# Optimization experiments

Hardware: AMD Instinct MI355X
Metric: run time of the kernel (lower is better)

The kernel has to match this reference:

```python
import jax, jax.numpy as jnp
import numpy as np

N_NODES = 35
N_EDGES = 1190
N_VIEWS = 6
C1_IN, C1_OUT = 1, 256
C2_IN, C2_OUT = 256, 256
C3_IN, C3_OUT = 256, 64


def _nnconv(x, edge_attr, src, dst, nn_w, nn_b, lin_w, bias, c_in, c_out):
    """PyG NNConv with aggr='mean': per-edge MLP weight, gather-matvec-scatter."""
    # per-edge weight matrices: [E, c_in, c_out]
    W = jax.nn.relu(edge_attr @ nn_w.T + nn_b).reshape(-1, c_in, c_out)
    # gather source features and apply per-edge weight: [E, c_out]
    msg = jnp.einsum('ei,eio->eo', x[src], W)
    # scatter-mean into target nodes
    agg = jax.ops.segment_sum(msg, dst, num_segments=N_NODES)
    cnt = jax.ops.segment_sum(jnp.ones((msg.shape[0],), msg.dtype), dst,
                              num_segments=N_NODES)
    agg = agg / jnp.maximum(cnt, 1.0)[:, None]
    # root transform (lin has no bias in PyG) + conv bias
    return agg + x @ lin_w.T + bias


def setup_inputs() -> dict:
    key = jax.random.key(0)
    ks = jax.random.split(key, 16)
    s = 0.05
    x = jnp.ones((N_NODES, C1_IN), jnp.float32)
    edge_attr = jax.random.uniform(ks[0], (N_EDGES, N_VIEWS), jnp.float32)
    edge_index = jax.random.randint(ks[1], (2, N_EDGES), 0, N_NODES, jnp.int32)
    inp = {
        'x': x, 'edge_attr': edge_attr, 'edge_index': edge_index,
        'nn1_w': jax.random.normal(ks[2], (C1_IN * C1_OUT, N_VIEWS), jnp.float32) * s,
        'nn1_b': jax.random.normal(ks[3], (C1_IN * C1_OUT,), jnp.float32) * s,
        'lin1_w': jax.random.normal(ks[4], (C1_OUT, C1_IN), jnp.float32) * s,
        'b1': jax.random.normal(ks[5], (C1_OUT,), jnp.float32) * s,
        'nn2_w': jax.random.normal(ks[6], (C2_IN * C2_OUT, N_VIEWS), jnp.float32) * s,
        'nn2_b': jax.random.normal(ks[7], (C2_IN * C2_OUT,), jnp.float32) * s,
        'lin2_w': jax.random.normal(ks[8], (C2_OUT, C2_IN), jnp.float32) * s,
        'b2': jax.random.normal(ks[9], (C2_OUT,), jnp.float32) * s,
        'nn3_w': jax.random.normal(ks[10], (C3_IN * C3_OUT, N_VIEWS), jnp.float32) * s,
        'nn3_b': jax.random.normal(ks[11], (C3_IN * C3_OUT,), jnp.float32) * s,
        'lin3_w': jax.random.normal(ks[12], (C3_OUT, C3_IN), jnp.float32) * s,
        'b3': jax.random.normal(ks[13], (C3_OUT,), jnp.float32) * s,
    }
    return inp


def reference(x, edge_attr, edge_index, nn1_w, nn1_b, lin1_w, b1,
              nn2_w, nn2_b, lin2_w, b2, nn3_w, nn3_b, lin3_w, b3):
    src, dst = edge_index[0], edge_index[1]
    x = jax.nn.relu(_nnconv(x, edge_attr, src, dst, nn1_w, nn1_b, lin1_w, b1, C1_IN, C1_OUT))
    x = jax.nn.relu(_nnconv(x, edge_attr, src, dst, nn2_w, nn2_b, lin2_w, b2, C2_IN, C2_OUT))
    x = jax.nn.relu(_nnconv(x, edge_attr, src, dst, nn3_w, nn3_b, lin3_w, b3, C3_IN, C3_OUT))
    # CBT: pairwise L1 distances over feature dim -> [N, N]
    # (equivalent to repeat(35,1,1) / transpose / abs / sum since N == 35)
    cbt = jnp.abs(x[None, :, :] - x[:, None, :]).sum(-1)
    return cbt
```

## Files before the change

### kernel.cpp

```cpp
#include <hip/hip_runtime.h>


#define NN 35
#define NE 1190
#define NBLK 224
#define MAXE 96

#define OFF_CNT  320
#define OFF_EL   384
#define OFF_X1   3840
#define OFF_X2   12800
#define OFF_X3   21760
#define OFF_AGG3 24064

__global__ __launch_bounds__(64) void init_k(unsigned* bar) {
    for (int i = threadIdx.x; i < 320; i += 64) bar[i] = 0u;
}

__device__ __forceinline__ float ld_c(const float* p) {
    return __hip_atomic_load(p, __ATOMIC_RELAXED, __HIP_MEMORY_SCOPE_AGENT);
}
__device__ __forceinline__ void st_c(float* p, float v) {
    __hip_atomic_store(p, v, __ATOMIC_RELAXED, __HIP_MEMORY_SCOPE_AGENT);
}
__device__ __forceinline__ int ld_ci(const int* p) {
    return __hip_atomic_load(p, __ATOMIC_RELAXED, __HIP_MEMORY_SCOPE_AGENT);
}
__device__ __forceinline__ void st_ci(int* p, int v) {
    __hip_atomic_store(p, v, __ATOMIC_RELAXED, __HIP_MEMORY_SCOPE_AGENT);
}
__device__ __forceinline__ float2 ld_c2(const float* p) {
    union { double d; float2 f; } u;
    u.d = __hip_atomic_load((const double*)p, __ATOMIC_RELAXED,
                            __HIP_MEMORY_SCOPE_AGENT);
    return u.f;
}
__device__ __forceinline__ void st_c2(float* p, float2 v) {
    union { double d; float2 f; } u;
    u.f = v;
    __hip_atomic_store((double*)p, u.d, __ATOMIC_RELAXED,
                       __HIP_MEMORY_SCOPE_AGENT);
}

__device__ __forceinline__ void gbar(unsigned* bar, unsigned target) {
    __syncthreads();
    if (threadIdx.x == 0) {
        __hip_atomic_fetch_add(bar + (blockIdx.x & 15) * 16, 1u,
                               __ATOMIC_RELAXED, __HIP_MEMORY_SCOPE_AGENT);
        for (;;) {
            unsigned s = 0;
#pragma unroll
            for (int i = 0; i < 16; i++)
                s += __hip_atomic_load(bar + i * 16, __ATOMIC_RELAXED,
                                       __HIP_MEMORY_SCOPE_AGENT);
            if (s >= target) break;
            __builtin_amdgcn_s_sleep(8);
        }
        asm volatile("" ::: "memory");
    }
    __syncthreads();
}

__global__ __launch_bounds__(512, 2) void mega_k(
    float* __restrict__ ws, const float* __restrict__ x,
    const float* __restrict__ ea, const int* __restrict__ ei,
    const float* __restrict__ w1, const float* __restrict__ b1w,
    const float* __restrict__ lin1, const float* __restrict__ b1,
    const float* __restrict__ w2, const float* __restrict__ b2w,
    const float* __restrict__ lin2, const float* __restrict__ b2,
    const float* __restrict__ w3, const float* __restrict__ b3w,
    const float* __restrict__ lin3, const float* __restrict__ b3,
    float* __restrict__ out) {
    __shared__ float smem[14400];
    unsigned* bar = (unsigned*)ws;
    const int tid = threadIdx.x;
    const int bid = blockIdx.x;

    if (bid < 140) {
        const int n = bid >> 2, och = bid & 3;
        int* elistS = (int*)smem;
        int* ecntS = (int*)smem + 96;
        float* partS = smem + 128;
        if (tid == 0) *ecntS = 0;
        __syncthreads();
        for (int e = tid; e < NE; e += 512) {
            if (ei[NE + e] == n) {
                const int p = atomicAdd(ecntS, 1);
                if (p < MAXE) elistS[p] = e;
            }
        }
        __syncthreads();
        const int deg = *ecntS;
        const int dl = deg < MAXE ? deg : MAXE;
        const int ol = tid & 63, ech = tid >> 6;
        const int o = och * 64 + ol;
        const float2* wr = (const float2*)(w1 + o * 6);
        const float2 wv0 = wr[0], wv1 = wr[1], wv2 = wr[2];
        const float bb = b1w[o];
        float a = 0.f;
        for (int k = ech; k < dl; k += 8) {
            const int e = elistS[k];
            const float2* eap = (const float2*)(ea + e * 6);
            const float2 a0 = eap[0], a1 = eap[1], a2 = eap[2];
            float d = bb;
            d = fmaf(a0.x, wv0.x, d); d = fmaf(a0.y, wv0.y, d);
            d = fmaf(a1.x, wv1.x, d); d = fmaf(a1.y, wv1.y, d);
            d = fmaf(a2.x, wv2.x, d); d = fmaf(a2.y, wv2.y, d);
            a = fmaf(x[ei[e]], fmaxf(d, 0.f), a);
        }
        partS[ech * 64 + ol] = a;
        __syncthreads();
        if (ech == 0) {
            float s = a;
#pragma unroll
            for (int p = 1; p < 8; p++) s += partS[p * 64 + ol];
            const float c = fmaxf((float)deg, 1.f);
            st_c(ws + OFF_X1 + n * 256 + o,
                 fmaxf(s / c + x[n] * lin1[o] + b1[o], 0.f));
        }
        if (och == 0) {
            if (tid < dl) st_ci((int*)(ws + OFF_EL) + n * MAXE + tid, elistS[tid]);
            if (tid == 0) st_c(ws + OFF_CNT + n, (float)deg);
        }
    } else {
        const int idx = (bid - 140) * 512 + tid;
        if (idx < NN * 64) st_c(ws + OFF_AGG3 + idx, 0.f);
    }
    gbar(bar, NBLK * 1u);

    {
        float* xsS = smem;
        float* x1S = smem + 12288;
        float* easS = smem + 12544;
        int* srcS = (int*)(smem + 13120);
        int* elS  = (int*)(smem + 13216);
        float* cS = smem + 13312;
        float* partA = smem + 13376;
        float* partB = smem + 13888;
        const int ol = tid & 15, ic = tid >> 4;
        for (int it = bid; it < NN * 16; it += NBLK) {
            const int n = it >> 4, og = it & 15;
            const int o = og * 16 + ol;
            __syncthreads();
            if (tid == 0) cS[0] = ld_c(ws + OFF_CNT + n);
            if (tid < MAXE)
                elS[tid] = ld_ci((const int*)(ws + OFF_EL) + n * MAXE + tid);
            if (tid >= 128 && tid < 256) {
                const int ip = (tid - 128) * 2;
                *(float2*)&x1S[ip] = ld_c2(ws + OFF_X1 + n * 256 + ip);
            }
            __syncthreads();
            const int deg = (int)cS[0];
            const int dl = deg < MAXE ? deg : MAXE;
            if (tid < dl) {
                const int eid = elS[tid];
                srcS[tid] = ei[eid];
                const float2* eap = (const float2*)(ea + eid * 6);
                *(float2*)&easS[tid * 6] = eap[0];
                *(float2*)&easS[tid * 6 + 2] = eap[1];
                *(float2*)&easS[tid * 6 + 4] = eap[2];
            }
            float accm = 0.f;
            for (int p = 0; p < 2; ++p) {
                __syncthreads();
                for (int idx = tid; idx < dl * 64; idx += 512) {
                    const int e = idx >> 6, ip = (idx & 63) * 2;
                    *(float2*)&xsS[e * 128 + ip] =
                        ld_c2(ws + OFF_X1 + srcS[e] * 256 + p * 128 + ip);
                }
                __syncthreads();
                const int i0 = p * 128 + ic * 4;
                const float* wp0 = w2 + (size_t)((i0 + 0) * 256 + o) * 6;
                const float* wp1 = w2 + (size_t)((i0 + 1) * 256 + o) * 6;
                const float* wp2 = w2 + (size_t)((i0 + 2) * 256 + o) * 6;
                const float* wp3 = w2 + (size_t)((i0 + 3) * 256 + o) * 6;
                const float2 wa0 = *(const float2*)wp0;
                const float2 wb0 = *(const float2*)(wp0 + 2);
                const float2 wc0 = *(const float2*)(wp0 + 4);
                const float2 wa1 = *(const float2*)wp1;
                const float2 wb1 = *(const float2*)(wp1 + 2);
                const float2 wc1 = *(const float2*)(wp1 + 4);
                const float2 wa2 = *(const float2*)wp2;
                const float2 wb2 = *(const float2*)(wp2 + 2);
                const float2 wc2 = *(const float2*)(wp2 + 4);
                const float2 wa3 = *(const float2*)wp3;
                const float2 wb3 = *(const float2*)(wp3 + 2);
                const float2 wc3 = *(const float2*)(wp3 + 4);
                const float bb0 = b2w[(i0 + 0) * 256 + o];
                const float bb1 = b2w[(i0 + 1) * 256 + o];
                const float bb2 = b2w[(i0 + 2) * 256 + o];
                const float bb3 = b2w[(i0 + 3) * 256 + o];
                for (int e = 0; e < dl; ++e) {
                    const float2 e01 = *(const float2*)&easS[e * 6];
                    const float2 e23 = *(const float2*)&easS[e * 6 + 2];
                    const float2 e45 = *(const float2*)&easS[e * 6 + 4];
                    const float4 xv = *(const float4*)&xsS[e * 128 + ic * 4];
                    float d0 = bb0, d1 = bb1, d2 = bb2, d3 = bb3;
                    d0 = fmaf(e01.x, wa0.x, d0); d1 = fmaf(e01.x, wa1.x, d1);
                    d2 = fmaf(e01.x, wa2.x, d2); d3 = fmaf(e01.x, wa3.x, d3);
                    d0 = fmaf(e01.y, wa0.y, d0); d1 = fmaf(e01.y, wa1.y, d1);
                    d2 = fmaf(e01.y, wa2.y, d2); d3 = fmaf(e01.y, wa3.y, d3);
                    d0 = fmaf(e23.x, wb0.x, d0); d1 = fmaf(e23.x, wb1.x, d1);
                    d2 = fmaf(e23.x, wb2.x, d2); d3 = fmaf(e23.x, wb3.x, d3);
                    d0 = fmaf(e23.y, wb0.y, d0); d1 = fmaf(e23.y, wb1.y, d1);
                    d2 = fmaf(e23.y, wb2.y, d2); d3 = fmaf(e23.y, wb3.y, d3);
                    d0 = fmaf(e45.x, wc0.x, d0); d1 = fmaf(e45.x, wc1.x, d1);
                    d2 = fmaf(e45.x, wc2.x, d2); d3 = fmaf(e45.x, wc3.x, d3);
                    d0 = fmaf(e45.y, wc0.y, d0); d1 = fmaf(e45.y, wc1.y, d1);
                    d2 = fmaf(e45.y, wc2.y, d2); d3 = fmaf(e45.y, wc3.y, d3);
                    d0 = fmaxf(d0, 0.f); d1 = fmaxf(d1, 0.f);
                    d2 = fmaxf(d2, 0.f); d3 = fmaxf(d3, 0.f);
                    accm = fmaf(xv.x, d0, accm);
                    accm = fmaf(xv.y, d1, accm);
                    accm = fmaf(xv.z, d2, accm);
                    accm = fmaf(xv.w, d3, accm);
                }
            }
            float accl = 0.f;
            {
                const float4 l0 = *(const float4*)(lin2 + (size_t)o * 256 + ic * 4);
                const float4 xa = *(const float4*)&x1S[ic * 4];
                accl = fmaf(l0.x, xa.x, accl); accl = fmaf(l0.y, xa.y, accl);
                accl = fmaf(l0.z, xa.z, accl); accl = fmaf(l0.w, xa.w, accl);
                const float4 l1 =
                    *(const float4*)(lin2 + (size_t)o * 256 + 128 + ic * 4);
                const float4 xb = *(const float4*)&x1S[128 + ic * 4];
                accl = fmaf(l1.x, xb.x, accl); accl = fmaf(l1.y, xb.y, accl);
                accl = fmaf(l1.z, xb.z, accl); accl = fmaf(l1.w, xb.w, accl);
            }
            partA[ic * 16 + ol] = accm;
            partB[ic * 16 + ol] = accl;
            __syncthreads();
            if (tid < 16) {
                float m = 0.f, l = 0.f;
                for (int k = 0; k < 32; ++k) {
                    m += partA[k * 16 + tid];
                    l += partB[k * 16 + tid];
                }
                const float c = fmaxf(cS[0], 1.f);
                st_c(ws + OFF_X2 + n * 256 + og * 16 + tid,
                     fmaxf(m / c + l + b2[og * 16 + tid], 0.f));
            }
        }
    }
    gbar(bar, NBLK * 2u);

    {
        float* xsS = smem;
        float* easS = smem + 3072;
        int* srcS = (int*)(smem + 3648);
        int* elS  = (int*)(smem + 3744);
        float* cS = smem + 3840;
        float* partS = smem + 3904;
        const int ol = tid & 63, ic = tid >> 6;
        for (int it = bid; it < NN * 8; it += NBLK) {
            const int n = it >> 3, iq = it & 7;
            const int i0 = iq * 32;
            __syncthreads();
            if (tid == 0) cS[0] = ld_c(ws + OFF_CNT + n);
            if (tid < MAXE)
                elS[tid] = ld_ci((const int*)(ws + OFF_EL) + n * MAXE + tid);
            __syncthreads();
            const int deg = (int)cS[0];
            const int dl = deg < MAXE ? deg : MAXE;
            if (tid < dl) {
                const int eid = elS[tid];
                srcS[tid] = ei[eid];
                const float2* eap = (const float2*)(ea + eid * 6);
                *(float2*)&easS[tid * 6] = eap[0];
                *(float2*)&easS[tid * 6 + 2] = eap[1];
                *(float2*)&easS[tid * 6 + 4] = eap[2];
            }
            __syncthreads();
            for (int idx = tid; idx < dl * 16; idx += 512) {
                const int e = idx >> 4, ip = (idx & 15) * 2;
                *(float2*)&xsS[e * 32 + ip] =
                    ld_c2(ws + OFF_X2 + srcS[e] * 256 + i0 + ip);
            }
            __syncthreads();
            const int ib = i0 + ic * 4;
            const float* wp0 = w3 + (size_t)((ib + 0) * 64 + ol) * 6;
            const float* wp1 = w3 + (size_t)((ib + 1) * 64 + ol) * 6;
            const float* wp2 = w3 + (size_t)((ib + 2) * 64 + ol) * 6;
            const float* wp3 = w3 + (size_t)((ib + 3) * 64 + ol) * 6;
            const float2 wa0 = *(const float2*)wp0;
            const float2 wb0 = *(const float2*)(wp0 + 2);
            const float2 wc0 = *(const float2*)(wp0 + 4);
            const float2 wa1 = *(const float2*)wp1;
            const float2 wb1 = *(const float2*)(wp1 + 2);
            const float2 wc1 = *(const float2*)(wp1 + 4);
            const float2 wa2 = *(const float2*)wp2;
            const float2 wb2 = *(const float2*)(wp2 + 2);
            const float2 wc2 = *(const float2*)(wp2 + 4);
            const float2 wa3 = *(const float2*)wp3;
            const float2 wb3 = *(const float2*)(wp3 + 2);
            const float2 wc3 = *(const float2*)(wp3 + 4);
            const float bb0 = b3w[(ib + 0) * 64 + ol];
            const float bb1 = b3w[(ib + 1) * 64 + ol];
            const float bb2 = b3w[(ib + 2) * 64 + ol];
            const float bb3 = b3w[(ib + 3) * 64 + ol];
            float accm = 0.f;
            for (int e = 0; e < dl; ++e) {
                const float2 e01 = *(const float2*)&easS[e * 6];
                const float2 e23 = *(const float2*)&easS[e * 6 + 2];
                const float2 e45 = *(const float2*)&easS[e * 6 + 4];
                const float4 xv = *(const float4*)&xsS[e * 32 + ic * 4];
                float d0 = bb0, d1 = bb1, d2 = bb2, d3 = bb3;
                d0 = fmaf(e01.x, wa0.x, d0); d1 = fmaf(e01.x, wa1.x, d1);
                d2 = fmaf(e01.x, wa2.x, d2); d3 = fmaf(e01.x, wa3.x, d3);
                d0 = fmaf(e01.y, wa0.y, d0); d1 = fmaf(e01.y, wa1.y, d1);
                d2 = fmaf(e01.y, wa2.y, d2); d3 = fmaf(e01.y, wa3.y, d3);
                d0 = fmaf(e23.x, wb0.x, d0); d1 = fmaf(e23.x, wb1.x, d1);
                d2 = fmaf(e23.x, wb2.x, d2); d3 = fmaf(e23.x, wb3.x, d3);
                d0 = fmaf(e23.y, wb0.y, d0); d1 = fmaf(e23.y, wb1.y, d1);
                d2 = fmaf(e23.y, wb2.y, d2); d3 = fmaf(e23.y, wb3.y, d3);
                d0 = fmaf(e45.x, wc0.x, d0); d1 = fmaf(e45.x, wc1.x, d1);
                d2 = fmaf(e45.x, wc2.x, d2); d3 = fmaf(e45.x, wc3.x, d3);
                d0 = fmaf(e45.y, wc0.y, d0); d1 = fmaf(e45.y, wc1.y, d1);
                d2 = fmaf(e45.y, wc2.y, d2); d3 = fmaf(e45.y, wc3.y, d3);
                d0 = fmaxf(d0, 0.f); d1 = fmaxf(d1, 0.f);
                d2 = fmaxf(d2, 0.f); d3 = fmaxf(d3, 0.f);
                accm = fmaf(xv.x, d0, accm);
                accm = fmaf(xv.y, d1, accm);
                accm = fmaf(xv.z, d2, accm);
                accm = fmaf(xv.w, d3, accm);
            }
            partS[ic * 64 + ol] = accm;
            __syncthreads();
            if (ic == 0) {
                float s = accm;
#pragma unroll
                for (int p = 1; p < 8; ++p) s += partS[p * 64 + ol];
                atomicAdd(ws + OFF_AGG3 + n * 64 + ol, s);
            }
        }
    }
    gbar(bar, NBLK * 3u);

    if (bid >= NN) return;
    {
        const int n = bid;
        float* x2S = smem;
        float* partS = smem + 256;
        float* cS = smem + 768;
        if (tid == 0) cS[0] = ld_c(ws + OFF_CNT + n);
        if (tid >= 128 && tid < 256) {
            const int ip = (tid - 128) * 2;
            *(float2*)&x2S[ip] = ld_c2(ws + OFF_X2 + n * 256 + ip);
        }
        __syncthreads();
        const int o3 = tid & 63, ic = tid >> 6;
        const float4* l4 = (const float4*)(lin3 + (size_t)o3 * 256 + ic * 32);
        const float* xs = x2S + ic * 32;
        float slin = 0.f;
#pragma unroll
        for (int k = 0; k < 8; k++) {
            const float4 wv = l4[k];
            slin = fmaf(wv.x, xs[k * 4], slin);
            slin = fmaf(wv.y, xs[k * 4 + 1], slin);
            slin = fmaf(wv.z, xs[k * 4 + 2], slin);
            slin = fmaf(wv.w, xs[k * 4 + 3], slin);
        }
        partS[ic * 64 + o3] = slin;
        __syncthreads();
        if (ic == 0) {
            float s = slin;
#pragma unroll
            for (int p = 1; p < 8; p++) s += partS[p * 64 + o3];
            const float g = ld_c(ws + OFF_AGG3 + n * 64 + o3);
            const float c = fmaxf(cS[0], 1.f);
            st_c(ws + OFF_X3 + n * 64 + o3, fmaxf(g / c + s + b3[o3], 0.f));
        }
        __syncthreads();
        if (tid == 0) {
            unsigned* flag = bar + 256;
            __hip_atomic_fetch_add(flag, 1u, __ATOMIC_RELAXED,
                                   __HIP_MEMORY_SCOPE_AGENT);
            while (__hip_atomic_load(flag, __ATOMIC_RELAXED,
                                     __HIP_MEMORY_SCOPE_AGENT) < NN)
                __builtin_amdgcn_s_sleep(4);
            asm volatile("" ::: "memory");
        }
        __syncthreads();
        float* sx = smem;
        for (int idx = tid; idx < NN * 32; idx += 512)
            *(float2*)&sx[idx * 2] = ld_c2(ws + OFF_X3 + idx * 2);
        __syncthreads();
        const int f = tid & 63, jg = tid >> 6;
        const float xi = sx[n * 64 + f];
        for (int j = jg; j < NN; j += 8) {
            float d = fabsf(xi - sx[j * 64 + f]);
#pragma unroll
            for (int off = 32; off > 0; off >>= 1) d += __shfl_xor(d, off);
            if (f == 0) out[n * NN + j] = d;
        }
    }
}

extern "C" void kernel_launch(void* const* d_in, const int* in_sizes, int n_in,
                              void* d_out, int out_size, void* d_ws, size_t ws_size,
                              hipStream_t stream) {
    (void)in_sizes; (void)n_in; (void)out_size; (void)ws_size;
    const float* x    = (const float*)d_in[0];
    const float* ea   = (const float*)d_in[1];
    const int*   ei   = (const int*)d_in[2];
    const float* nn1w = (const float*)d_in[3];
    const float* nn1b = (const float*)d_in[4];
    const float* lin1 = (const float*)d_in[5];
    const float* b1   = (const float*)d_in[6];
    const float* nn2w = (const float*)d_in[7];
    const float* nn2b = (const float*)d_in[8];
    const float* lin2 = (const float*)d_in[9];
    const float* b2   = (const float*)d_in[10];
    const float* nn3w = (const float*)d_in[11];
    const float* nn3b = (const float*)d_in[12];
    const float* lin3 = (const float*)d_in[13];
    const float* b3   = (const float*)d_in[14];

    float* ws = (float*)d_ws;
    init_k<<<1, 64, 0, stream>>>((unsigned*)d_ws);
    mega_k<<<NBLK, 512, 0, stream>>>(ws, x, ea, ei, nn1w, nn1b, lin1, b1,
                                     nn2w, nn2b, lin2, b2, nn3w, nn3b,
                                     lin3, b3, (float*)d_out);
}
```

Before: 147.2 us.

## Split persistent megakernel into five kernel launches instead of software grid barriers

Replaces the single persistent kernel, which used atomic-counter grid barriers and a flag spin-wait, with five separate kernels: layer 1, layer 2, layer 3 messages, layer 3 finalize, and CBT. Stream ordering now provides the stage boundaries, which removes the spin-wait barrier cost and the relaxed atomic loads and stores, so plain vectorized float4 accesses can be used. Each stage also launches its own full grid instead of looping over a fixed 224 blocks, and MAXE drops from 96 to 80 to shrink shared memory. The trade is extra launch overhead for each of the four added kernels, and any node with more than 80 incoming edges would now be truncated.

```diff
diff --git a/kernel.cpp b/kernel.cpp
--- a/kernel.cpp
+++ b/kernel.cpp
@@ -3,397 +3,328 @@
 
 #define NN 35
 #define NE 1190
-#define NBLK 224
-#define MAXE 96
-
-#define OFF_CNT  320
-#define OFF_EL   384
-#define OFF_X1   3840
-#define OFF_X2   12800
-#define OFF_X3   21760
-#define OFF_AGG3 24064
-
-__global__ __launch_bounds__(64) void init_k(unsigned* bar) {
-    for (int i = threadIdx.x; i < 320; i += 64) bar[i] = 0u;
-}
-
-__device__ __forceinline__ float ld_c(const float* p) {
-    return __hip_atomic_load(p, __ATOMIC_RELAXED, __HIP_MEMORY_SCOPE_AGENT);
-}
-__device__ __forceinline__ void st_c(float* p, float v) {
-    __hip_atomic_store(p, v, __ATOMIC_RELAXED, __HIP_MEMORY_SCOPE_AGENT);
-}
-__device__ __forceinline__ int ld_ci(const int* p) {
-    return __hip_atomic_load(p, __ATOMIC_RELAXED, __HIP_MEMORY_SCOPE_AGENT);
-}
-__device__ __forceinline__ void st_ci(int* p, int v) {
-    __hip_atomic_store(p, v, __ATOMIC_RELAXED, __HIP_MEMORY_SCOPE_AGENT);
-}
-__device__ __forceinline__ float2 ld_c2(const float* p) {
-    union { double d; float2 f; } u;
-    u.d = __hip_atomic_load((const double*)p, __ATOMIC_RELAXED,
-                            __HIP_MEMORY_SCOPE_AGENT);
-    return u.f;
-}
-__device__ __forceinline__ void st_c2(float* p, float2 v) {
-    union { double d; float2 f; } u;
-    u.f = v;
-    __hip_atomic_store((double*)p, u.d, __ATOMIC_RELAXED,
-                       __HIP_MEMORY_SCOPE_AGENT);
-}
-
-__device__ __forceinline__ void gbar(unsigned* bar, unsigned target) {
-    __syncthreads();
-    if (threadIdx.x == 0) {
-        __hip_atomic_fetch_add(bar + (blockIdx.x & 15) * 16, 1u,
-                               __ATOMIC_RELAXED, __HIP_MEMORY_SCOPE_AGENT);
-        for (;;) {
-            unsigned s = 0;
-#pragma unroll
-            for (int i = 0; i < 16; i++)
-                s += __hip_atomic_load(bar + i * 16, __ATOMIC_RELAXED,
-                                       __HIP_MEMORY_SCOPE_AGENT);
-            if (s >= target) break;
-            __builtin_amdgcn_s_sleep(8);
-        }
-        asm volatile("" ::: "memory");
-    }
-    __syncthreads();
-}
-
-__global__ __launch_bounds__(512, 2) void mega_k(
+#define MAXE 80
+
+#define OFF_CNT  0
+#define OFF_EL   64
+#define OFF_X1   2944
+#define OFF_X2   11904
+#define OFF_X3   20864
+#define OFF_AGG3 23168
+
+__global__ __launch_bounds__(512) void x1_k(
     float* __restrict__ ws, const float* __restrict__ x,
     const float* __restrict__ ea, const int* __restrict__ ei,
     const float* __restrict__ w1, const float* __restrict__ b1w,
-    const float* __restrict__ lin1, const float* __restrict__ b1,
-    const float* __restrict__ w2, const float* __restrict__ b2w,
-    const float* __restrict__ lin2, const float* __restrict__ b2,
-    const float* __restrict__ w3, const float* __restrict__ b3w,
-    const float* __restrict__ lin3, const float* __restrict__ b3,
-    float* __restrict__ out) {
-    __shared__ float smem[14400];
-    unsigned* bar = (unsigned*)ws;
+    const float* __restrict__ lin1, const float* __restrict__ b1) {
+    __shared__ int elistS[MAXE];
+    __shared__ int ecntS;
+    __shared__ float partS[8 * 64];
+    const int tid = threadIdx.x, bid = blockIdx.x;
+    if (bid >= 140) {
+        const int idx = (bid - 140) * 512 + tid;
+        if (idx < NN * 64) ws[OFF_AGG3 + idx] = 0.f;
+        return;
+    }
+    const int n = bid >> 2, och = bid & 3;
+    if (tid == 0) ecntS = 0;
+    __syncthreads();
+    for (int e = tid; e < NE; e += 512) {
+        if (ei[NE + e] == n) {
+            const int p = atomicAdd(&ecntS, 1);
+            if (p < MAXE) elistS[p] = e;
+        }
+    }
+    __syncthreads();
+    const int deg = ecntS;
+    const int dl = deg < MAXE ? deg : MAXE;
+    const int ol = tid & 63, ech = tid >> 6;
+    const int o = och * 64 + ol;
+    const float2* wr = (const float2*)(w1 + o * 6);
+    const float2 wv0 = wr[0], wv1 = wr[1], wv2 = wr[2];
+    const float bb = b1w[o];
+    float a = 0.f;
+    for (int k = ech; k < dl; k += 8) {
+        const int e = elistS[k];
+        const float2* eap = (const float2*)(ea + e * 6);
+        const float2 a0 = eap[0], a1 = eap[1], a2 = eap[2];
+        float d = bb;
+        d = fmaf(a0.x, wv0.x, d); d = fmaf(a0.y, wv0.y, d);
+        d = fmaf(a1.x, wv1.x, d); d = fmaf(a1.y, wv1.y, d);
+        d = fmaf(a2.x, wv2.x, d); d = fmaf(a2.y, wv2.y, d);
+        a = fmaf(x[ei[e]], fmaxf(d, 0.f), a);
+    }
+    partS[ech * 64 + ol] = a;
+    __syncthreads();
+    if (ech == 0) {
+        float s = a;
+#pragma unroll
+        for (int p = 1; p < 8; p++) s += partS[p * 64 + ol];
+        const float c = fmaxf((float)deg, 1.f);
+        ws[OFF_X1 + n * 256 + o] = fmaxf(s / c + x[n] * lin1[o] + b1[o], 0.f);
+    }
+    if (och == 0) {
+        if (tid < dl) ((int*)(ws + OFF_EL))[n * MAXE + tid] = elistS[tid];
+        if (tid == 0) ws[OFF_CNT + n] = (float)deg;
+    }
+}
+
+__global__ __launch_bounds__(512) void x2_k(
+    float* __restrict__ ws, const float* __restrict__ ea,
+    const int* __restrict__ ei, const float* __restrict__ w2,
+    const float* __restrict__ b2w, const float* __restrict__ lin2,
+    const float* __restrict__ b2) {
+    __shared__ float smem[11264];
+    float* xsS = smem;
+    float* x1S = smem + 10240;
+    float* easS = smem + 10496;
+    int* srcS = (int*)(smem + 10976);
+    int* elS = (int*)(smem + 11056);
+    float* partA = smem;
+    float* partB = smem + 512;
+    __shared__ float cS;
     const int tid = threadIdx.x;
-    const int bid = blockIdx.x;
-
-    if (bid < 140) {
-        const int n = bid >> 2, och = bid & 3;
-        int* elistS = (int*)smem;
-        int* ecntS = (int*)smem + 96;
-        float* partS = smem + 128;
-        if (tid == 0) *ecntS = 0;
+    const int n = blockIdx.x >> 4, og = blockIdx.x & 15;
+    const int ol = tid & 15, ic = tid >> 4;
+    const int o = og * 16 + ol;
+    if (tid == 0) cS = ws[OFF_CNT + n];
+    if (tid < MAXE) elS[tid] = ((const int*)(ws + OFF_EL))[n * MAXE + tid];
+    if (tid >= 448) {
+        const int q = tid - 448;
+        *(float4*)&x1S[q * 4] = *(const float4*)(ws + OFF_X1 + n * 256 + q * 4);
+    }
+    __syncthreads();
+    const int deg = (int)cS;
+    const int dl = deg < MAXE ? deg : MAXE;
+    if (tid < dl) {
+        const int eid = elS[tid];
+        srcS[tid] = ei[eid];
+        const float2* eap = (const float2*)(ea + eid * 6);
+        *(float2*)&easS[tid * 6] = eap[0];
+        *(float2*)&easS[tid * 6 + 2] = eap[1];
+        *(float2*)&easS[tid * 6 + 4] = eap[2];
+    }
+    float accm = 0.f;
+    for (int p = 0; p < 2; ++p) {
         __syncthreads();
-        for (int e = tid; e < NE; e += 512) {
-            if (ei[NE + e] == n) {
-                const int p = atomicAdd(ecntS, 1);
-                if (p < MAXE) elistS[p] = e;
-            }
+        for (int idx = tid; idx < dl * 32; idx += 512) {
+            const int e = idx >> 5, ip = (idx & 31) * 4;
+            *(float4*)&xsS[e * 128 + ip] =
+                *(const float4*)(ws + OFF_X1 + srcS[e] * 256 + p * 128 + ip);
         }
         __syncthreads();
-        const int deg = *ecntS;
-        const int dl = deg < MAXE ? deg : MAXE;
-        const int ol = tid & 63, ech = tid >> 6;
-        const int o = och * 64 + ol;
-        const float2* wr = (const float2*)(w1 + o * 6);
-        const float2 wv0 = wr[0], wv1 = wr[1], wv2 = wr[2];
-        const float bb = b1w[o];
-        float a = 0.f;
-        for (int k = ech; k < dl; k += 8) {
-            const int e = elistS[k];
-            const float2* eap = (const float2*)(ea + e * 6);
-            const float2 a0 = eap[0], a1 = eap[1], a2 = eap[2];
-            float d = bb;
-            d = fmaf(a0.x, wv0.x, d); d = fmaf(a0.y, wv0.y, d);
-            d = fmaf(a1.x, wv1.x, d); d = fmaf(a1.y, wv1.y, d);
-            d = fmaf(a2.x, wv2.x, d); d = fmaf(a2.y, wv2.y, d);
-            a = fmaf(x[ei[e]], fmaxf(d, 0.f), a);
+        const int i0 = p * 128 + ic * 4;
+        const float* wp0 = w2 + (size_t)((i0 + 0) * 256 + o) * 6;
+        const float* wp1 = w2 + (size_t)((i0 + 1) * 256 + o) * 6;
+        const float* wp2 = w2 + (size_t)((i0 + 2) * 256 + o) * 6;
+        const float* wp3 = w2 + (size_t)((i0 + 3) * 256 + o) * 6;
+        const float2 wa0 = *(const float2*)wp0;
+        const float2 wb0 = *(const float2*)(wp0 + 2);
+        const float2 wc0 = *(const float2*)(wp0 + 4);
+        const float2 wa1 = *(const float2*)wp1;
+        const float2 wb1 = *(const float2*)(wp1 + 2);
+        const float2 wc1 = *(const float2*)(wp1 + 4);
+        const float2 wa2 = *(const float2*)wp2;
+        const float2 wb2 = *(const float2*)(wp2 + 2);
+        const float2 wc2 = *(const float2*)(wp2 + 4);
+        const float2 wa3 = *(const float2*)wp3;
+        const float2 wb3 = *(const float2*)(wp3 + 2);
+        const float2 wc3 = *(const float2*)(wp3 + 4);
+        const float bb0 = b2w[(i0 + 0) * 256 + o];
+        const float bb1 = b2w[(i0 + 1) * 256 + o];
+        const float bb2 = b2w[(i0 + 2) * 256 + o];
+        const float bb3 = b2w[(i0 + 3) * 256 + o];
+        for (int e = 0; e < dl; ++e) {
+            const float2 e01 = *(const float2*)&easS[e * 6];
+            const float2 e23 = *(const float2*)&easS[e * 6 + 2];
+            const float2 e45 = *(const float2*)&easS[e * 6 + 4];
+            const float4 xv = *(const float4*)&xsS[e * 128 + ic * 4];
+            float d0 = bb0, d1 = bb1, d2 = bb2, d3 = bb3;
+            d0 = fmaf(e01.x, wa0.x, d0); d1 = fmaf(e01.x, wa1.x, d1);
+            d2 = fmaf(e01.x, wa2.x, d2); d3 = fmaf(e01.x, wa3.x, d3);
+            d0 = fmaf(e01.y, wa0.y, d0); d1 = fmaf(e01.y, wa1.y, d1);
+            d2 = fmaf(e01.y, wa2.y, d2); d3 = fmaf(e01.y, wa3.y, d3);
+            d0 = fmaf(e23.x, wb0.x, d0); d1 = fmaf(e23.x, wb1.x, d1);
+            d2 = fmaf(e23.x, wb2.x, d2); d3 = fmaf(e23.x, wb3.x, d3);
+            d0 = fmaf(e23.y, wb0.y, d0); d1 = fmaf(e23.y, wb1.y, d1);
+            d2 = fmaf(e23.y, wb2.y, d2); d3 = fmaf(e23.y, wb3.y, d3);
+            d0 = fmaf(e45.x, wc0.x, d0); d1 = fmaf(e45.x, wc1.x, d1);
+            d2 = fmaf(e45.x, wc2.x, d2); d3 = fmaf(e45.x, wc3.x, d3);
+            d0 = fmaf(e45.y, wc0.y, d0); d1 = fmaf(e45.y, wc1.y, d1);
+            d2 = fmaf(e45.y, wc2.y, d2); d3 = fmaf(e45.y, wc3.y, d3);
+            d0 = fmaxf(d0, 0.f); d1 = fmaxf(d1, 0.f);
+            d2 = fmaxf(d2, 0.f); d3 = fmaxf(d3, 0.f);
+            accm = fmaf(xv.x, d0, accm);
+            accm = fmaf(xv.y, d1, accm);
+            accm = fmaf(xv.z, d2, accm);
+            accm = fmaf(xv.w, d3, accm);
         }
-        partS[ech * 64 + ol] = a;
-        __syncthreads();
-        if (ech == 0) {
-            float s = a;
+    }
+    float accl = 0.f;
+    {
+        const float4 l0 = *(const float4*)(lin2 + (size_t)o * 256 + ic * 4);
+        const float4 xa = *(const float4*)&x1S[ic * 4];
+        accl = fmaf(l0.x, xa.x, accl); accl = fmaf(l0.y, xa.y, accl);
+        accl = fmaf(l0.z, xa.z, accl); accl = fmaf(l0.w, xa.w, accl);
+        const float4 l1 = *(const float4*)(lin2 + (size_t)o * 256 + 128 + ic * 4);
+        const float4 xb = *(const float4*)&x1S[128 + ic * 4];
+        accl = fmaf(l1.x, xb.x, accl); accl = fmaf(l1.y, xb.y, accl);
+        accl = fmaf(l1.z, xb.z, accl); accl = fmaf(l1.w, xb.w, accl);
+    }
+    __syncthreads();
+    partA[ic * 16 + ol] = accm;
+    partB[ic * 16 + ol] = accl;
+    __syncthreads();
+    if (tid < 16) {
+        float m = 0.f, l = 0.f;
+        for (int k = 0; k < 32; ++k) {
+            m += partA[k * 16 + tid];
+            l += partB[k * 16 + tid];
+        }
+        const float c = fmaxf(cS, 1.f);
+        ws[OFF_X2 + n * 256 + og * 16 + tid] =
+            fmaxf(m / c + l + b2[og * 16 + tid], 0.f);
+    }
+}
+
+__global__ __launch_bounds__(512) void p3_k(
+    float* __restrict__ ws, const float* __restrict__ ea,
+    const int* __restrict__ ei, const float* __restrict__ w3,
+    const float* __restrict__ b3w) {
+    __shared__ float xsS[MAXE * 32];
+    __shared__ float easS[MAXE * 6];
+    __shared__ int srcS[MAXE];
+    __shared__ int elS[MAXE];
+    __shared__ float partS[8 * 64];
+    __shared__ float cS;
+    const int tid = threadIdx.x;
+    const int n = blockIdx.x >> 3, iq = blockIdx.x & 7;
+    const int i0 = iq * 32;
+    const int ol = tid & 63, ic = tid >> 6;
+    if (tid == 0) cS = ws[OFF_CNT + n];
+    if (tid < MAXE) elS[tid] = ((const int*)(ws + OFF_EL))[n * MAXE + tid];
+    __syncthreads();
+    const int deg = (int)cS;
+    const int dl = deg < MAXE ? deg : MAXE;
+    if (tid < dl) {
+        const int eid = elS[tid];
+        srcS[tid] = ei[eid];
+        const float2* eap = (const float2*)(ea + eid * 6);
+        *(float2*)&easS[tid * 6] = eap[0];
+        *(float2*)&easS[tid * 6 + 2] = eap[1];
+        *(float2*)&easS[tid * 6 + 4] = eap[2];
+    }
+    __syncthreads();
+    for (int idx = tid; idx < dl * 8; idx += 512) {
+        const int e = idx >> 3, ip = (idx & 7) * 4;
+        *(float4*)&xsS[e * 32 + ip] =
+            *(const float4*)(ws + OFF_X2 + srcS[e] * 256 + i0 + ip);
+    }
+    __syncthreads();
+    const int ib = i0 + ic * 4;
+    const float* wp0 = w3 + (size_t)((ib + 0) * 64 + ol) * 6;
+    const float* wp1 = w3 + (size_t)((ib + 1) * 64 + ol) * 6;
+    const float* wp2 = w3 + (size_t)((ib + 2) * 64 + ol) * 6;
+    const float* wp3 = w3 + (size_t)((ib + 3) * 64 + ol) * 6;
+    const float2 wa0 = *(const float2*)wp0;
+    const float2 wb0 = *(const float2*)(wp0 + 2);
+    const float2 wc0 = *(const float2*)(wp0 + 4);
+    const float2 wa1 = *(const float2*)wp1;
+    const float2 wb1 = *(const float2*)(wp1 + 2);
+    const float2 wc1 = *(const float2*)(wp1 + 4);
+    const float2 wa2 = *(const float2*)wp2;
+    const float2 wb2 = *(const float2*)(wp2 + 2);
+    const float2 wc2 = *(const float2*)(wp2 + 4);
+    const float2 wa3 = *(const float2*)wp3;
+    const float2 wb3 = *(const float2*)(wp3 + 2);
+    const float2 wc3 = *(const float2*)(wp3 + 4);
+    const float bb0 = b3w[(ib + 0) * 64 + ol];
+    const float bb1 = b3w[(ib + 1) * 64 + ol];
+    const float bb2 = b3w[(ib + 2) * 64 + ol];
+    const float bb3 = b3w[(ib + 3) * 64 + ol];
+    float accm = 0.f;
+    for (int e = 0; e < dl; ++e) {
+        const float2 e01 = *(const float2*)&easS[e * 6];
+        const float2 e23 = *(const float2*)&easS[e * 6 + 2];
+        const float2 e45 = *(const float2*)&easS[e * 6 + 4];
+        const float4 xv = *(const float4*)&xsS[e * 32 + ic * 4];
+        float d0 = bb0, d1 = bb1, d2 = bb2, d3 = bb3;
+        d0 = fmaf(e01.x, wa0.x, d0); d1 = fmaf(e01.x, wa1.x, d1);
+        d2 = fmaf(e01.x, wa2.x, d2); d3 = fmaf(e01.x, wa3.x, d3);
+        d0 = fmaf(e01.y, wa0.y, d0); d1 = fmaf(e01.y, wa1.y, d1);
+        d2 = fmaf(e01.y, wa2.y, d2); d3 = fmaf(e01.y, wa3.y, d3);
+        d0 = fmaf(e23.x, wb0.x, d0); d1 = fmaf(e23.x, wb1.x, d1);
+        d2 = fmaf(e23.x, wb2.x, d2); d3 = fmaf(e23.x, wb3.x, d3);
+        d0 = fmaf(e23.y, wb0.y, d0); d1 = fmaf(e23.y, wb1.y, d1);
+        d2 = fmaf(e23.y, wb2.y, d2); d3 = fmaf(e23.y, wb3.y, d3);
+        d0 = fmaf(e45.x, wc0.x, d0); d1 = fmaf(e45.x, wc1.x, d1);
+        d2 = fmaf(e45.x, wc2.x, d2); d3 = fmaf(e45.x, wc3.x, d3);
+        d0 = fmaf(e45.y, wc0.y, d0); d1 = fmaf(e45.y, wc1.y, d1);
+        d2 = fmaf(e45.y, wc2.y, d2); d3 = fmaf(e45.y, wc3.y, d3);
+        d0 = fmaxf(d0, 0.f); d1 = fmaxf(d1, 0.f);
+        d2 = fmaxf(d2, 0.f); d3 = fmaxf(d3, 0.f);
+        accm = fmaf(xv.x, d0, accm);
+        accm = fmaf(xv.y, d1, accm);
+        accm = fmaf(xv.z, d2, accm);
+        accm = fmaf(xv.w, d3, accm);
+    }
+    partS[ic * 64 + ol] = accm;
+    __syncthreads();
+    if (ic == 0) {
+        float s = accm;
 #pragma unroll
-            for (int p = 1; p < 8; p++) s += partS[p * 64 + ol];
-            const float c = fmaxf((float)deg, 1.f);
-            st_c(ws + OFF_X1 + n * 256 + o,
-                 fmaxf(s / c + x[n] * lin1[o] + b1[o], 0.f));
-        }
-        if (och == 0) {
-            if (tid < dl) st_ci((int*)(ws + OFF_EL) + n * MAXE + tid, elistS[tid]);
-            if (tid == 0) st_c(ws + OFF_CNT + n, (float)deg);
-        }
-    } else {
-        const int idx = (bid - 140) * 512 + tid;
-        if (idx < NN * 64) st_c(ws + OFF_AGG3 + idx, 0.f);
-    }
-    gbar(bar, NBLK * 1u);
-
-    {
-        float* xsS = smem;
-        float* x1S = smem + 12288;
-        float* easS = smem + 12544;
-        int* srcS = (int*)(smem + 13120);
-        int* elS  = (int*)(smem + 13216);
-        float* cS = smem + 13312;
-        float* partA = smem + 13376;
-        float* partB = smem + 13888;
-        const int ol = tid & 15, ic = tid >> 4;
-        for (int it = bid; it < NN * 16; it += NBLK) {
-            const int n = it >> 4, og = it & 15;
-            const int o = og * 16 + ol;
-            __syncthreads();
-            if (tid == 0) cS[0] = ld_c(ws + OFF_CNT + n);
-            if (tid < MAXE)
-                elS[tid] = ld_ci((const int*)(ws + OFF_EL) + n * MAXE + tid);
-            if (tid >= 128 && tid < 256) {
-                const int ip = (tid - 128) * 2;
-                *(float2*)&x1S[ip] = ld_c2(ws + OFF_X1 + n * 256 + ip);
-            }
-            __syncthreads();
-            const int deg = (int)cS[0];
-            const int dl = deg < MAXE ? deg : MAXE;
-            if (tid < dl) {
-                const int eid = elS[tid];
-                srcS[tid] = ei[eid];
-                const float2* eap = (const float2*)(ea + eid * 6);
-                *(float2*)&easS[tid * 6] = eap[0];
-                *(float2*)&easS[tid * 6 + 2] = eap[1];
-                *(float2*)&easS[tid * 6 + 4] = eap[2];
-            }
-            float accm = 0.f;
-            for (int p = 0; p < 2; ++p) {
-                __syncthreads();
-                for (int idx = tid; idx < dl * 64; idx += 512) {
-                    const int e = idx >> 6, ip = (idx & 63) * 2;
-                    *(float2*)&xsS[e * 128 + ip] =
-                        ld_c2(ws + OFF_X1 + srcS[e] * 256 + p * 128 + ip);
-                }
-                __syncthreads();
-                const int i0 = p * 128 + ic * 4;
-                const float* wp0 = w2 + (size_t)((i0 + 0) * 256 + o) * 6;
-                const float* wp1 = w2 + (size_t)((i0 + 1) * 256 + o) * 6;
-                const float* wp2 = w2 + (size_t)((i0 + 2) * 256 + o) * 6;
-                const float* wp3 = w2 + (size_t)((i0 + 3) * 256 + o) * 6;
-                const float2 wa0 = *(const float2*)wp0;
-                const float2 wb0 = *(const float2*)(wp0 + 2);
-                const float2 wc0 = *(const float2*)(wp0 + 4);
-                const float2 wa1 = *(const float2*)wp1;
-                const float2 wb1 = *(const float2*)(wp1 + 2);
-                const float2 wc1 = *(const float2*)(wp1 + 4);
-                const float2 wa2 = *(const float2*)wp2;
-                const float2 wb2 = *(const float2*)(wp2 + 2);
-                const float2 wc2 = *(const float2*)(wp2 + 4);
-                const float2 wa3 = *(const float2*)wp3;
-                const float2 wb3 = *(const float2*)(wp3 + 2);
-                const float2 wc3 = *(const float2*)(wp3 + 4);
-                const float bb0 = b2w[(i0 + 0) * 256 + o];
-                const float bb1 = b2w[(i0 + 1) * 256 + o];
-                const float bb2 = b2w[(i0 + 2) * 256 + o];
-                const float bb3 = b2w[(i0 + 3) * 256 + o];
-                for (int e = 0; e < dl; ++e) {
-                    const float2 e01 = *(const float2*)&easS[e * 6];
-                    const float2 e23 = *(const float2*)&easS[e * 6 + 2];
-                    const float2 e45 = *(const float2*)&easS[e * 6 + 4];
-                    const float4 xv = *(const float4*)&xsS[e * 128 + ic * 4];
-                    float d0 = bb0, d1 = bb1, d2 = bb2, d3 = bb3;
-                    d0 = fmaf(e01.x, wa0.x, d0); d1 = fmaf(e01.x, wa1.x, d1);
-                    d2 = fmaf(e01.x, wa2.x, d2); d3 = fmaf(e01.x, wa3.x, d3);
-                    d0 = fmaf(e01.y, wa0.y, d0); d1 = fmaf(e01.y, wa1.y, d1);
-                    d2 = fmaf(e01.y, wa2.y, d2); d3 = fmaf(e01.y, wa3.y, d3);
-                    d0 = fmaf(e23.x, wb0.x, d0); d1 = fmaf(e23.x, wb1.x, d1);
-                    d2 = fmaf(e23.x, wb2.x, d2); d3 = fmaf(e23.x, wb3.x, d3);
-                    d0 = fmaf(e23.y, wb0.y, d0); d1 = fmaf(e23.y, wb1.y, d1);
-                    d2 = fmaf(e23.y, wb2.y, d2); d3 = fmaf(e23.y, wb3.y, d3);
-                    d0 = fmaf(e45.x, wc0.x, d0); d1 = fmaf(e45.x, wc1.x, d1);
-                    d2 = fmaf(e45.x, wc2.x, d2); d3 = fmaf(e45.x, wc3.x, d3);
-                    d0 = fmaf(e45.y, wc0.y, d0); d1 = fmaf(e45.y, wc1.y, d1);
-                    d2 = fmaf(e45.y, wc2.y, d2); d3 = fmaf(e45.y, wc3.y, d3);
-                    d0 = fmaxf(d0, 0.f); d1 = fmaxf(d1, 0.f);
-                    d2 = fmaxf(d2, 0.f); d3 = fmaxf(d3, 0.f);
-                    accm = fmaf(xv.x, d0, accm);
-                    accm = fmaf(xv.y, d1, accm);
-                    accm = fmaf(xv.z, d2, accm);
-                    accm = fmaf(xv.w, d3, accm);
-                }
-            }
-            float accl = 0.f;
-            {
-                const float4 l0 = *(const float4*)(lin2 + (size_t)o * 256 + ic * 4);
-                const float4 xa = *(const float4*)&x1S[ic * 4];
-                accl = fmaf(l0.x, xa.x, accl); accl = fmaf(l0.y, xa.y, accl);
-                accl = fmaf(l0.z, xa.z, accl); accl = fmaf(l0.w, xa.w, accl);
-                const float4 l1 =
-                    *(const float4*)(lin2 + (size_t)o * 256 + 128 + ic * 4);
-                const float4 xb = *(const float4*)&x1S[128 + ic * 4];
-                accl = fmaf(l1.x, xb.x, accl); accl = fmaf(l1.y, xb.y, accl);
-                accl = fmaf(l1.z, xb.z, accl); accl = fmaf(l1.w, xb.w, accl);
-            }
-            partA[ic * 16 + ol] = accm;
-            partB[ic * 16 + ol] = accl;
-            __syncthreads();
-            if (tid < 16) {
-                float m = 0.f, l = 0.f;
-                for (int k = 0; k < 32; ++k) {
-                    m += partA[k * 16 + tid];
-                    l += partB[k * 16 + tid];
-                }
-                const float c = fmaxf(cS[0], 1.f);
-                st_c(ws + OFF_X2 + n * 256 + og * 16 + tid,
-                     fmaxf(m / c + l + b2[og * 16 + tid], 0.f));
-            }
-        }
-    }
-    gbar(bar, NBLK * 2u);
-
-    {
-        float* xsS = smem;
-        float* easS = smem + 3072;
-        int* srcS = (int*)(smem + 3648);
-        int* elS  = (int*)(smem + 3744);
-        float* cS = smem + 3840;
-        float* partS = smem + 3904;
-        const int ol = tid & 63, ic = tid >> 6;
-        for (int it = bid; it < NN * 8; it += NBLK) {
-            const int n = it >> 3, iq = it & 7;
-            const int i0 = iq * 32;
-            __syncthreads();
-            if (tid == 0) cS[0] = ld_c(ws + OFF_CNT + n);
-            if (tid < MAXE)
-                elS[tid] = ld_ci((const int*)(ws + OFF_EL) + n * MAXE + tid);
-            __syncthreads();
-            const int deg = (int)cS[0];
-            const int dl = deg < MAXE ? deg : MAXE;
-            if (tid < dl) {
-                const int eid = elS[tid];
-                srcS[tid] = ei[eid];
-                const float2* eap = (const float2*)(ea + eid * 6);
-                *(float2*)&easS[tid * 6] = eap[0];
-                *(float2*)&easS[tid * 6 + 2] = eap[1];
-                *(float2*)&easS[tid * 6 + 4] = eap[2];
-            }
-            __syncthreads();
-            for (int idx = tid; idx < dl * 16; idx += 512) {
-                const int e = idx >> 4, ip = (idx & 15) * 2;
-                *(float2*)&xsS[e * 32 + ip] =
-                    ld_c2(ws + OFF_X2 + srcS[e] * 256 + i0 + ip);
-            }
-            __syncthreads();
-            const int ib = i0 + ic * 4;
-            const float* wp0 = w3 + (size_t)((ib + 0) * 64 + ol) * 6;
-            const float* wp1 = w3 + (size_t)((ib + 1) * 64 + ol) * 6;
-            const float* wp2 = w3 + (size_t)((ib + 2) * 64 + ol) * 6;
-            const float* wp3 = w3 + (size_t)((ib + 3) * 64 + ol) * 6;
-            const float2 wa0 = *(const float2*)wp0;
-            const float2 wb0 = *(const float2*)(wp0 + 2);
-            const float2 wc0 = *(const float2*)(wp0 + 4);
-            const float2 wa1 = *(const float2*)wp1;
-            const float2 wb1 = *(const float2*)(wp1 + 2);
-            const float2 wc1 = *(const float2*)(wp1 + 4);
-            const float2 wa2 = *(const float2*)wp2;
-            const float2 wb2 = *(const float2*)(wp2 + 2);
-            const float2 wc2 = *(const float2*)(wp2 + 4);
-            const float2 wa3 = *(const float2*)wp3;
-            const float2 wb3 = *(const float2*)(wp3 + 2);
-            const float2 wc3 = *(const float2*)(wp3 + 4);
-            const float bb0 = b3w[(ib + 0) * 64 + ol];
-            const float bb1 = b3w[(ib + 1) * 64 + ol];
-            const float bb2 = b3w[(ib + 2) * 64 + ol];
-            const float bb3 = b3w[(ib + 3) * 64 + ol];
-            float accm = 0.f;
-            for (int e = 0; e < dl; ++e) {
-                const float2 e01 = *(const float2*)&easS[e * 6];
-                const float2 e23 = *(const float2*)&easS[e * 6 + 2];
-                const float2 e45 = *(const float2*)&easS[e * 6 + 4];
-                const float4 xv = *(const float4*)&xsS[e * 32 + ic * 4];
-                float d0 = bb0, d1 = bb1, d2 = bb2, d3 = bb3;
-                d0 = fmaf(e01.x, wa0.x, d0); d1 = fmaf(e01.x, wa1.x, d1);
-                d2 = fmaf(e01.x, wa2.x, d2); d3 = fmaf(e01.x, wa3.x, d3);
-                d0 = fmaf(e01.y, wa0.y, d0); d1 = fmaf(e01.y, wa1.y, d1);
-                d2 = fmaf(e01.y, wa2.y, d2); d3 = fmaf(e01.y, wa3.y, d3);
-                d0 = fmaf(e23.x, wb0.x, d0); d1 = fmaf(e23.x, wb1.x, d1);
-                d2 = fmaf(e23.x, wb2.x, d2); d3 = fmaf(e23.x, wb3.x, d3);
-                d0 = fmaf(e23.y, wb0.y, d0); d1 = fmaf(e23.y, wb1.y, d1);
-                d2 = fmaf(e23.y, wb2.y, d2); d3 = fmaf(e23.y, wb3.y, d3);
-                d0 = fmaf(e45.x, wc0.x, d0); d1 = fmaf(e45.x, wc1.x, d1);
-                d2 = fmaf(e45.x, wc2.x, d2); d3 = fmaf(e45.x, wc3.x, d3);
-                d0 = fmaf(e45.y, wc0.y, d0); d1 = fmaf(e45.y, wc1.y, d1);
-                d2 = fmaf(e45.y, wc2.y, d2); d3 = fmaf(e45.y, wc3.y, d3);
-                d0 = fmaxf(d0, 0.f); d1 = fmaxf(d1, 0.f);
-                d2 = fmaxf(d2, 0.f); d3 = fmaxf(d3, 0.f);
-                accm = fmaf(xv.x, d0, accm);
-                accm = fmaf(xv.y, d1, accm);
-                accm = fmaf(xv.z, d2, accm);
-                accm = fmaf(xv.w, d3, accm);
-            }
-            partS[ic * 64 + ol] = accm;
-            __syncthreads();
-            if (ic == 0) {
-                float s = accm;
+        for (int p = 1; p < 8; ++p) s += partS[p * 64 + ol];
+        atomicAdd(ws + OFF_AGG3 + n * 64 + ol, s);
+    }
+}
+
+__global__ __launch_bounds__(256) void x3_k(float* __restrict__ ws,
+                                            const float* __restrict__ lin3,
+                                            const float* __restrict__ b3) {
+    __shared__ float x2S[256];
+    __shared__ float partS[3 * 64];
+    __shared__ float cS;
+    const int n = blockIdx.x, tid = threadIdx.x;
+    const int o3 = tid & 63, ic = tid >> 6;
+    if (tid == 0) cS = ws[OFF_CNT + n];
+    if (tid < 64)
+        *(float4*)&x2S[tid * 4] = *(const float4*)(ws + OFF_X2 + n * 256 + tid * 4);
+    __syncthreads();
+    const float4* l4 = (const float4*)(lin3 + (size_t)o3 * 256 + ic * 64);
+    float s = 0.f;
 #pragma unroll
-                for (int p = 1; p < 8; ++p) s += partS[p * 64 + ol];
-                atomicAdd(ws + OFF_AGG3 + n * 64 + ol, s);
-            }
-        }
-    }
-    gbar(bar, NBLK * 3u);
-
-    if (bid >= NN) return;
-    {
-        const int n = bid;
-        float* x2S = smem;
-        float* partS = smem + 256;
-        float* cS = smem + 768;
-        if (tid == 0) cS[0] = ld_c(ws + OFF_CNT + n);
-        if (tid >= 128 && tid < 256) {
-            const int ip = (tid - 128) * 2;
-            *(float2*)&x2S[ip] = ld_c2(ws + OFF_X2 + n * 256 + ip);
-        }
-        __syncthreads();
-        const int o3 = tid & 63, ic = tid >> 6;
-        const float4* l4 = (const float4*)(lin3 + (size_t)o3 * 256 + ic * 32);
-        const float* xs = x2S + ic * 32;
-        float slin = 0.f;
+    for (int k = 0; k < 16; k++) {
+        const float4 wv = l4[k];
+        const int i = ic * 64 + k * 4;
+        s = fmaf(wv.x, x2S[i], s);
+        s = fmaf(wv.y, x2S[i + 1], s);
+        s = fmaf(wv.z, x2S[i + 2], s);
+        s = fmaf(wv.w, x2S[i + 3], s);
+    }
+    if (ic > 0) partS[(ic - 1) * 64 + o3] = s;
+    __syncthreads();
+    if (ic == 0) {
+        const float tot = s + partS[o3] + partS[64 + o3] + partS[128 + o3];
+        const float c = fmaxf(cS, 1.f);
+        ws[OFF_X3 + n * 64 + o3] =
+            fmaxf(ws[OFF_AGG3 + n * 64 + o3] / c + tot + b3[o3], 0.f);
+    }
+}
+
+__global__ __launch_bounds__(512) void cbt_k(const float* __restrict__ ws,
+                                             float* __restrict__ out) {
+    __shared__ float sx[NN * 64];
+    const int tid = threadIdx.x;
+    for (int idx = tid; idx < NN * 16; idx += 512)
+        *(float4*)&sx[idx * 4] = *(const float4*)(ws + OFF_X3 + idx * 4);
+    __syncthreads();
+    const int f = tid & 63, jg = tid >> 6;
+    const float xi = sx[blockIdx.x * 64 + f];
+    for (int j = jg; j < NN; j += 8) {
+        float d = fabsf(xi - sx[j * 64 + f]);
 #pragma unroll
-        for (int k = 0; k < 8; k++) {
-            const float4 wv = l4[k];
-            slin = fmaf(wv.x, xs[k * 4], slin);
-            slin = fmaf(wv.y, xs[k * 4 + 1], slin);
-            slin = fmaf(wv.z, xs[k * 4 + 2], slin);
-            slin = fmaf(wv.w, xs[k * 4 + 3], slin);
-        }
-        partS[ic * 64 + o3] = slin;
-        __syncthreads();
-        if (ic == 0) {
-            float s = slin;
-#pragma unroll
-            for (int p = 1; p < 8; p++) s += partS[p * 64 + o3];
-            const float g = ld_c(ws + OFF_AGG3 + n * 64 + o3);
-            const float c = fmaxf(cS[0], 1.f);
-            st_c(ws + OFF_X3 + n * 64 + o3, fmaxf(g / c + s + b3[o3], 0.f));
-        }
-        __syncthreads();
-        if (tid == 0) {
-            unsigned* flag = bar + 256;
-            __hip_atomic_fetch_add(flag, 1u, __ATOMIC_RELAXED,
-                                   __HIP_MEMORY_SCOPE_AGENT);
-            while (__hip_atomic_load(flag, __ATOMIC_RELAXED,
-                                     __HIP_MEMORY_SCOPE_AGENT) < NN)
-                __builtin_amdgcn_s_sleep(4);
-            asm volatile("" ::: "memory");
-        }
-        __syncthreads();
-        float* sx = smem;
-        for (int idx = tid; idx < NN * 32; idx += 512)
-            *(float2*)&sx[idx * 2] = ld_c2(ws + OFF_X3 + idx * 2);
-        __syncthreads();
-        const int f = tid & 63, jg = tid >> 6;
-        const float xi = sx[n * 64 + f];
-        for (int j = jg; j < NN; j += 8) {
-            float d = fabsf(xi - sx[j * 64 + f]);
-#pragma unroll
-            for (int off = 32; off > 0; off >>= 1) d += __shfl_xor(d, off);
-            if (f == 0) out[n * NN + j] = d;
-        }
+        for (int off = 32; off > 0; off >>= 1) d += __shfl_xor(d, off);
+        if (f == 0) out[blockIdx.x * NN + j] = d;
     }
 }
 
@@ -418,8 +349,9 @@
     const float* b3   = (const float*)d_in[14];
 
     float* ws = (float*)d_ws;
-    init_k<<<1, 64, 0, stream>>>((unsigned*)d_ws);
-    mega_k<<<NBLK, 512, 0, stream>>>(ws, x, ea, ei, nn1w, nn1b, lin1, b1,
-                                     nn2w, nn2b, lin2, b2, nn3w, nn3b,
-                                     lin3, b3, (float*)d_out);
-}
+    x1_k<<<145, 512, 0, stream>>>(ws, x, ea, ei, nn1w, nn1b, lin1, b1);
+    x2_k<<<NN * 16, 512, 0, stream>>>(ws, ea, ei, nn2w, nn2b, lin2, b2);
+    p3_k<<<NN * 8, 512, 0, stream>>>(ws, ea, ei, nn3w, nn3b);
+    x3_k<<<NN, 256, 0, stream>>>(ws, lin3, b3);
+    cbt_k<<<NN, 512, 0, stream>>>(ws, (float*)d_out);
+}
```

Result: faster. 126.0 us (-14.4%).
